# Optimization experiments

Hardware: AMD Instinct MI355X
Metric: run time of the kernel (lower is better)

The kernel has to match this reference:

```python
import jax, jax.numpy as jnp
import numpy as np

N = 50000
E = 800000
H = 128

def _mlp_init(key, sizes, bias_flags):
    ws = []
    for i, (din, dout) in enumerate(zip(sizes[:-1], sizes[1:])):
        key, k1, k2 = jax.random.split(key, 3)
        lim = 1.0 / np.sqrt(din)
        W = jax.random.uniform(k1, (din, dout), jnp.float32, -lim, lim)
        ws.append(W)
        if bias_flags[i]:
            ws.append(jax.random.uniform(k2, (dout,), jnp.float32, -lim, lim))
    return key, ws

def setup_inputs() -> dict:
    key = jax.random.key(0)
    key, kh, kx, ke = jax.random.split(key, 4)
    h = jax.random.normal(kh, (N, H), jnp.float32)
    x = jax.random.normal(kx, (N, 3), jnp.float32)
    edge_index = jax.random.randint(ke, (2, E), 0, N, jnp.int64)
    # edge_mlp: Linear(2H+1, H), Linear(H, H), both with bias
    key, (W_e1, b_e1, W_e2, b_e2) = _mlp_init(key, [2 * H + 1, H, H], [True, True])
    # coord_mlp: Linear(H, H) with bias, Linear(H, 1) no bias
    key, (W_c1, b_c1, W_c2) = _mlp_init(key, [H, H, 1], [True, False])
    # node_mlp: Linear(2H, H), Linear(H, H), both with bias
    key, (W_n1, b_n1, W_n2, b_n2) = _mlp_init(key, [2 * H, H, H], [True, True])
    ln_g = jnp.ones((H,), jnp.float32)
    ln_b = jnp.zeros((H,), jnp.float32)
    return {"h": h, "x": x, "edge_index": edge_index,
            "W_e1": W_e1, "b_e1": b_e1, "W_e2": W_e2, "b_e2": b_e2,
            "W_c1": W_c1, "b_c1": b_c1, "W_c2": W_c2,
            "W_n1": W_n1, "b_n1": b_n1, "W_n2": W_n2, "b_n2": b_n2,
            "ln_g": ln_g, "ln_b": ln_b}

def reference(h, x, edge_index, W_e1, b_e1, W_e2, b_e2, W_c1, b_c1, W_c2,
              W_n1, b_n1, W_n2, b_n2, ln_g, ln_b):
    row, col = edge_index[0], edge_index[1]
    coord_diff = x[row] - x[col]                       # [E, 3]
    dist = jnp.linalg.norm(coord_diff, axis=1, keepdims=True)  # [E, 1]
    radial = dist ** 2
    edge_input = jnp.concatenate([h[row], h[col], radial], axis=1)  # [E, 2H+1]
    m_ij = jax.nn.silu(jax.nn.silu(edge_input @ W_e1 + b_e1) @ W_e2 + b_e2)  # [E, H]
    force_scalar = jnp.tanh(jax.nn.silu(m_ij @ W_c1 + b_c1) @ W_c2) * 0.1    # [E, 1]
    norm_diff = coord_diff / (dist + 1e-8)
    force_vector = norm_diff * force_scalar            # [E, 3]
    x_new = x + jax.ops.segment_sum(force_vector, row, num_segments=N)
    m_i = jax.ops.segment_sum(m_ij, row, num_segments=N)  # [N, H]
    node_input = jnp.concatenate([h, m_i], axis=1)     # [N, 2H]
    h_res = h + jax.nn.silu(node_input @ W_n1 + b_n1) @ W_n2 + b_n2
    mu = jnp.mean(h_res, axis=-1, keepdims=True)
    var = jnp.var(h_res, axis=-1, keepdims=True)
    h_new = (h_res - mu) / jnp.sqrt(var + 1e-5) * ln_g + ln_b
    return (h_new, x_new)
```

## Files before the change

kernel.cpp:

```cpp
#include <hip/hip_runtime.h>
#include <hip/hip_bf16.h>

#define NN 50000
#define NE 800000
#define HH 128
#define SCAN_NB 196

typedef short s16x8 __attribute__((ext_vector_type(8)));
typedef float f32x4 __attribute__((ext_vector_type(4)));
typedef unsigned int u32x4 __attribute__((ext_vector_type(4)));
typedef __bf16 bf16x2 __attribute__((ext_vector_type(2)));

__device__ __forceinline__ float u2f(unsigned int v) {
    float f;
    __builtin_memcpy(&f, &v, 4);
    return f;
}
__device__ __forceinline__ float bf2f(unsigned short u) {
    return u2f(((unsigned int)u) << 16);
}
__device__ __forceinline__ unsigned short f2bf_sw(float f) {
    unsigned int x;
    __builtin_memcpy(&x, &f, 4);
    unsigned int r = (x + 0x7fffu + ((x >> 16) & 1u)) >> 16;
    return (unsigned short)r;
}
__device__ __forceinline__ unsigned int f2bf_pk(float a, float b) {
#if __has_builtin(__builtin_amdgcn_cvt_pk_bf16_f32)
    bf16x2 p = __builtin_amdgcn_cvt_pk_bf16_f32(a, b);
    unsigned int u;
    __builtin_memcpy(&u, &p, 4);
    return u;
#else
    return (unsigned int)f2bf_sw(a) | ((unsigned int)f2bf_sw(b) << 16);
#endif
}
__device__ __forceinline__ unsigned short f2bf(float a) {
#if __has_builtin(__builtin_amdgcn_cvt_pk_bf16_f32)
    return (unsigned short)(f2bf_pk(a, a) & 0xffffu);
#else
    return f2bf_sw(a);
#endif
}
__device__ __forceinline__ float silu(float v) {
    return v * __builtin_amdgcn_rcpf(1.f + __expf(-v));
}

__global__ void prep_kernel(
    const float* __restrict__ W_e1, const float* __restrict__ W_e2,
    const float* __restrict__ W_c1, const float* __restrict__ W_n1,
    const float* __restrict__ W_n2, const int* __restrict__ eidx,
    unsigned short* __restrict__ PWT, unsigned short* __restrict__ W2T,
    unsigned short* __restrict__ Wc1T, unsigned short* __restrict__ Wn1T,
    unsigned short* __restrict__ Wn2T, int* __restrict__ counts) {
    int idx = blockIdx.x * 256 + threadIdx.x;
    if (idx < 32768) {
        int cp = idx >> 7, k = idx & 127;
        int srow = (cp < 128) ? k : (128 + k);
        PWT[idx] = f2bf(W_e1[srow * 128 + (cp & 127)]);
    } else if (idx < 49152) {
        int i = idx - 32768, n = i >> 7, k = i & 127;
        W2T[i] = f2bf(W_e2[k * 128 + n]);
    } else if (idx < 65536) {
        int i = idx - 49152, n = i >> 7, k = i & 127;
        Wc1T[i] = f2bf(W_c1[k * 128 + n]);
    } else if (idx < 98304) {
        int i = idx - 65536, n = i >> 8, k = i & 255;
        Wn1T[i] = f2bf(W_n1[k * 128 + n]);
    } else if (idx < 114688) {
        int i = idx - 98304, n = i >> 7, k = i & 127;
        Wn2T[i] = f2bf(W_n2[k * 128 + n]);
    } else if (idx < 114688 + NE) {
        int e = idx - 114688;
        int r = eidx[e];
        r = r < 0 ? 0 : (r >= NN ? NN - 1 : r);
        atomicAdd(&counts[r], 1);
    }
}

__global__ void k_partial(const int* __restrict__ counts, int* __restrict__ partials) {
    __shared__ int sm[256];
    int idx = blockIdx.x * 256 + threadIdx.x;
    sm[threadIdx.x] = idx < NN ? counts[idx] : 0;
    __syncthreads();
    for (int s = 128; s > 0; s >>= 1) {
        if (threadIdx.x < s) sm[threadIdx.x] += sm[threadIdx.x + s];
        __syncthreads();
    }
    if (threadIdx.x == 0) partials[blockIdx.x] = sm[0];
}
__global__ void k_scanp(const int* __restrict__ partials, int* __restrict__ scanp) {
    __shared__ int sm[256];
    int t = threadIdx.x;
    int v = t < SCAN_NB ? partials[t] : 0;
    sm[t] = v;
    __syncthreads();
    for (int d = 1; d < 256; d <<= 1) {
        int add = t >= d ? sm[t - d] : 0;
        __syncthreads();
        sm[t] += add;
        __syncthreads();
    }
    scanp[t] = sm[t] - v;
}
__global__ void k_offsets(const int* __restrict__ counts, const int* __restrict__ scanp,
                          int* __restrict__ offsets) {
    __shared__ int sm[256];
    int t = threadIdx.x, idx = blockIdx.x * 256 + t;
    int v = idx < NN ? counts[idx] : 0;
    sm[t] = v;
    __syncthreads();
    for (int d = 1; d < 256; d <<= 1) {
        int add = t >= d ? sm[t - d] : 0;
        __syncthreads();
        sm[t] += add;
        __syncthreads();
    }
    if (idx < NN) offsets[idx] = sm[t] - v + scanp[blockIdx.x];
}

__global__ void k_fill(const int* __restrict__ eidx, const int* __restrict__ offsets,
                       int* __restrict__ cursor, unsigned int* __restrict__ rc) {
    int e = blockIdx.x * 256 + threadIdx.x;
    if (e >= NE) return;
    int r = eidx[e];
    int c = eidx[NE + e];
    r = r < 0 ? 0 : (r >= NN ? NN - 1 : r);
    c = c < 0 ? 0 : (c >= NN ? NN - 1 : c);
    int slot = offsets[r] + atomicAdd(&cursor[r], 1);
    rc[slot] = (unsigned int)r | ((unsigned int)c << 16);
}

__global__ __launch_bounds__(256, 4) void pgemm(
    const float* __restrict__ h, const unsigned short* __restrict__ PWT,
    const float* __restrict__ b1,
    float* __restrict__ P1, float* __restrict__ P2) {
    __shared__ unsigned short Alds[64 * 136];
    const int tid = threadIdx.x;
    const int n0 = blockIdx.x * 64;

#pragma unroll
    for (int j = 0; j < 4; j++) {
        int idx = tid + j * 256;
        int e = idx >> 4, ch = idx & 15;
        int node = n0 + e;
        if (node >= NN) node = NN - 1;
        const f32x4* p = (const f32x4*)&h[node * 128 + ch * 8];
        f32x4 a = p[0], b = p[1];
        u32x4 s;
        s[0] = f2bf_pk(a[0], a[1]);
        s[1] = f2bf_pk(a[2], a[3]);
        s[2] = f2bf_pk(b[0], b[1]);
        s[3] = f2bf_pk(b[2], b[3]);
        *(u32x4*)&Alds[e * 136 + ch * 8] = s;
    }
    __syncthreads();

    const int lane = tid & 63;
    const int w = tid >> 6;
    const int ln15 = lane & 15;
    const int q8 = (lane >> 4) * 8, q4 = (lane >> 4) * 4;
    const int cbase = w * 64;

    f32x4 acc[4][4];
#pragma unroll
    for (int et = 0; et < 4; et++)
#pragma unroll
        for (int nt = 0; nt < 4; nt++) acc[et][nt] = (f32x4){0.f, 0.f, 0.f, 0.f};
#pragma unroll
    for (int kk = 0; kk < 4; kk++) {
        int k0 = kk * 32 + q8;
        s16x8 a[4], b[4];
#pragma unroll
        for (int et = 0; et < 4; et++)
            a[et] = *(const s16x8*)&Alds[(et * 16 + ln15) * 136 + k0];
#pragma unroll
        for (int nt = 0; nt < 4; nt++)
            b[nt] = *(const s16x8*)&PWT[(cbase + nt * 16 + ln15) * 128 + k0];
#pragma unroll
        for (int et = 0; et < 4; et++)
#pragma unroll
            for (int nt = 0; nt < 4; nt++)
                acc[et][nt] = __builtin_amdgcn_mfma_f32_16x16x32_bf16(
                    a[et], b[nt], acc[et][nt], 0, 0, 0);
    }
#pragma unroll
    for (int nt = 0; nt < 4; nt++) {
        int cp = cbase + nt * 16 + ln15;
        bool top = cp < 128;
        float* dst = top ? P1 : P2;
        int col = cp & 127;
        float badd = top ? b1[col] : 0.f;
#pragma unroll
        for (int et = 0; et < 4; et++)
#pragma unroll
            for (int r = 0; r < 4; r++) {
                int row = et * 16 + q4 + r;
                int node = n0 + row;
                if (node >= NN) node = NN - 1;
                dst[(size_t)node * 128 + col] = acc[et][nt][r] + badd;
            }
    }
}

__global__ __launch_bounds__(256, 8) void edge_kernel(
    const float* __restrict__ P1, const float* __restrict__ P2,
    const float* __restrict__ x, const unsigned int* __restrict__ rc,
    const float* __restrict__ W1full,
    const unsigned short* __restrict__ W2T, const float* __restrict__ b2,
    const unsigned short* __restrict__ Wc1T, const float* __restrict__ bc1,
    const float* __restrict__ wc2,
    float* __restrict__ m_i, float* __restrict__ x_acc) {
    __shared__ unsigned short mid1[64 * 132];
    __shared__ float wls[128];
    __shared__ float rad[64], ndx[64], ndy[64], ndz[64], fsum[64];
    __shared__ int rowA[64], colA[64];

    const int tid = threadIdx.x;
    const int e0 = blockIdx.x * 64;

    if (tid < 64) {
        unsigned int pk = rc[e0 + tid];
        int r = pk & 0xffff, c = pk >> 16;
        rowA[tid] = r; colA[tid] = c;
        float dx = x[r * 3 + 0] - x[c * 3 + 0];
        float dy = x[r * 3 + 1] - x[c * 3 + 1];
        float dz = x[r * 3 + 2] - x[c * 3 + 2];
        float d2 = dx * dx + dy * dy + dz * dz;
        float dist = sqrtf(d2);
        float inv = __builtin_amdgcn_rcpf(dist + 1e-8f);
        rad[tid] = d2;
        ndx[tid] = dx * inv; ndy[tid] = dy * inv; ndz[tid] = dz * inv;
        fsum[tid] = 0.f;
    } else if (tid >= 128 && tid < 256) {
        int c = tid - 128;
        wls[c] = W1full[256 * 128 + c];
    }
    __syncthreads();

#pragma unroll
    for (int j = 0; j < 4; j++) {
        int idx = tid + j * 256;
        int e = idx >> 4, ch = idx & 15;
        int r = rowA[e], c = colA[e];
        const f32x4* q1 = (const f32x4*)&P1[(size_t)r * 128 + ch * 8];
        const f32x4* q2 = (const f32x4*)&P2[(size_t)c * 128 + ch * 8];
        f32x4 a0 = q1[0], a1 = q1[1];
        f32x4 c0 = q2[0], c1 = q2[1];
        float rd = rad[e];
        int colb = ch * 8;
        u32x4 s;
#pragma unroll
        for (int t = 0; t < 2; t++) {
            float v0 = a0[t * 2] + c0[t * 2] + rd * wls[colb + t * 2];
            float v1 = a0[t * 2 + 1] + c0[t * 2 + 1] + rd * wls[colb + t * 2 + 1];
            s[t] = f2bf_pk(silu(v0), silu(v1));
        }
#pragma unroll
        for (int t = 0; t < 2; t++) {
            int cc = colb + 4 + t * 2;
            float v0 = a1[t * 2] + c1[t * 2] + rd * wls[cc];
            float v1 = a1[t * 2 + 1] + c1[t * 2 + 1] + rd * wls[cc + 1];
            s[t + 2] = f2bf_pk(silu(v0), silu(v1));
        }
        *(u32x4*)&mid1[e * 132 + ch * 8] = s;
    }
    __syncthreads();

    const int lane = tid & 63;
    const int w = tid >> 6;
    const int ln15 = lane & 15;
    const int q8 = (lane >> 4) * 8, q4 = (lane >> 4) * 4;
    const int nbase = w * 32;

    f32x4 acc[4][2];

#pragma unroll
    for (int et = 0; et < 4; et++)
#pragma unroll
        for (int nt = 0; nt < 2; nt++) acc[et][nt] = (f32x4){0.f, 0.f, 0.f, 0.f};
#pragma unroll
    for (int kk = 0; kk < 4; kk++) {
        int k0 = kk * 32 + q8;
        s16x8 a[4], b[2];
#pragma unroll
        for (int et = 0; et < 4; et++)
            a[et] = *(const s16x8*)&mid1[(et * 16 + ln15) * 132 + k0];
#pragma unroll
        for (int nt = 0; nt < 2; nt++)
            b[nt] = *(const s16x8*)&W2T[(nbase + nt * 16 + ln15) * 128 + k0];
#pragma unroll
        for (int et = 0; et < 4; et++)
#pragma unroll
            for (int nt = 0; nt < 2; nt++)
                acc[et][nt] = __builtin_amdgcn_mfma_f32_16x16x32_bf16(
                    a[et], b[nt], acc[et][nt], 0, 0, 0);
    }
    __syncthreads();
    unsigned short* mid2 = mid1;
#pragma unroll
    for (int nt = 0; nt < 2; nt++) {
        int col = nbase + nt * 16 + ln15;
        float bias = b2[col];
#pragma unroll
        for (int et = 0; et < 4; et++)
#pragma unroll
            for (int r = 0; r < 4; r++) {
                int row = et * 16 + q4 + r;
                mid2[row * 132 + col] = f2bf(silu(acc[et][nt][r] + bias));
            }
    }
    __syncthreads();

#pragma unroll
    for (int et = 0; et < 4; et++)
#pragma unroll
        for (int nt = 0; nt < 2; nt++) acc[et][nt] = (f32x4){0.f, 0.f, 0.f, 0.f};
#pragma unroll
    for (int kk = 0; kk < 4; kk++) {
        int k0 = kk * 32 + q8;
        s16x8 a[4], b[2];
#pragma unroll
        for (int et = 0; et < 4; et++)
            a[et] = *(const s16x8*)&mid2[(et * 16 + ln15) * 132 + k0];
#pragma unroll
        for (int nt = 0; nt < 2; nt++)
            b[nt] = *(const s16x8*)&Wc1T[(nbase + nt * 16 + ln15) * 128 + k0];
#pragma unroll
        for (int et = 0; et < 4; et++)
#pragma unroll
            for (int nt = 0; nt < 2; nt++)
                acc[et][nt] = __builtin_amdgcn_mfma_f32_16x16x32_bf16(
                    a[et], b[nt], acc[et][nt], 0, 0, 0);
    }

    {
        int cp2 = (tid & 63) * 2;
        int g = tid >> 6;
        int r0 = g * 16;
        float a0 = 0.f, a1 = 0.f;
        int cur = rowA[r0];
        for (int row = r0; row < r0 + 16; row++) {
            int rn = rowA[row];
            if (rn != cur) {
                atomicAdd(&m_i[(size_t)cur * 128 + cp2], a0);
                atomicAdd(&m_i[(size_t)cur * 128 + cp2 + 1], a1);
                a0 = 0.f; a1 = 0.f;
                cur = rn;
            }
            unsigned int v = *(const unsigned int*)&mid2[row * 132 + cp2];
            a0 += u2f(v << 16);
            a1 += u2f(v & 0xffff0000u);
        }
        atomicAdd(&m_i[(size_t)cur * 128 + cp2], a0);
        atomicAdd(&m_i[(size_t)cur * 128 + cp2 + 1], a1);
    }

    {
        float part[4][4];
#pragma unroll
        for (int et = 0; et < 4; et++)
#pragma unroll
            for (int r = 0; r < 4; r++) part[et][r] = 0.f;
#pragma unroll
        for (int nt = 0; nt < 2; nt++) {
            int col = nbase + nt * 16 + ln15;
            float bias = bc1[col];
            float w2 = wc2[col];
#pragma unroll
            for (int et = 0; et < 4; et++)
#pragma unroll
                for (int r = 0; r < 4; r++)
                    part[et][r] += silu(acc[et][nt][r] + bias) * w2;
        }
#pragma unroll
        for (int et = 0; et < 4; et++)
#pragma unroll
            for (int r = 0; r < 4; r++) {
                float p = part[et][r];
                p += __shfl_xor(p, 8, 16);
                p += __shfl_xor(p, 4, 16);
                p += __shfl_xor(p, 2, 16);
                p += __shfl_xor(p, 1, 16);
                if (ln15 == 0) atomicAdd(&fsum[et * 16 + q4 + r], p);
            }
    }
    __syncthreads();
    if (tid < 64) {
        float fs = tanhf(fsum[tid]) * 0.1f;
        ndx[tid] *= fs; ndy[tid] *= fs; ndz[tid] *= fs;
    }
    __syncthreads();
    if (tid < 64) {
        bool head = (tid == 0) || (rowA[tid] != rowA[tid - 1]);
        if (head) {
            int rn = rowA[tid];
            float ax = 0.f, ay = 0.f, az = 0.f;
            for (int j = tid; j < 64 && rowA[j] == rn; j++) {
                ax += ndx[j]; ay += ndy[j]; az += ndz[j];
            }
            atomicAdd(&x_acc[rn * 3 + 0], ax);
            atomicAdd(&x_acc[rn * 3 + 1], ay);
            atomicAdd(&x_acc[rn * 3 + 2], az);
        }
    }
}

__global__ __launch_bounds__(256, 4) void node_kernel(
    const float* __restrict__ h, const float* __restrict__ m_i,
    const float* __restrict__ x, const float* __restrict__ x_acc,
    const unsigned short* __restrict__ Wn1T, const float* __restrict__ bn1,
    const unsigned short* __restrict__ Wn2T, const float* __restrict__ bn2,
    const float* __restrict__ ln_g, const float* __restrict__ ln_b,
    float* __restrict__ out_h, float* __restrict__ out_x) {
    __shared__ unsigned short Alds[64 * 264];
    unsigned short* mid1 = Alds;
    float* tile = (float*)Alds;

    const int tid = threadIdx.x;
    const int n0 = blockIdx.x * 64;

    if (tid < 192) {
        int i = n0 * 3 + tid;
        if (i < NN * 3) out_x[i] = x[i] + x_acc[i];
    }

#pragma unroll
    for (int i = 0; i < 8; i++) {
        int idx = tid + i * 256;
        int hr = idx >> 4, ch = idx & 15;
        int e = hr >> 1, half = hr & 1;
        int node = n0 + e;
        if (node >= NN) node = NN - 1;
        const float* src = half ? &m_i[(size_t)node * 128 + ch * 8]
                                : &h[(size_t)node * 128 + ch * 8];
        const f32x4* sp = (const f32x4*)src;
        f32x4 f0 = sp[0], f1 = sp[1];
        u32x4 s;
        s[0] = f2bf_pk(f0[0], f0[1]);
        s[1] = f2bf_pk(f0[2], f0[3]);
        s[2] = f2bf_pk(f1[0], f1[1]);
        s[3] = f2bf_pk(f1[2], f1[3]);
        *(u32x4*)&Alds[e * 264 + half * 128 + ch * 8] = s;
    }
    __syncthreads();

    const int lane = tid & 63;
    const int w = tid >> 6;
    const int ln15 = lane & 15;
    const int q8 = (lane >> 4) * 8, q4 = (lane >> 4) * 4;
    const int nbase = w * 32;

    f32x4 acc[4][2];

#pragma unroll
    for (int et = 0; et < 4; et++)
#pragma unroll
        for (int nt = 0; nt < 2; nt++) acc[et][nt] = (f32x4){0.f, 0.f, 0.f, 0.f};
#pragma unroll
    for (int kk = 0; kk < 8; kk++) {
        int k0 = kk * 32 + q8;
        s16x8 a[4], b[2];
#pragma unroll
        for (int et = 0; et < 4; et++)
            a[et] = *(const s16x8*)&Alds[(et * 16 + ln15) * 264 + k0];
#pragma unroll
        for (int nt = 0; nt < 2; nt++)
            b[nt] = *(const s16x8*)&Wn1T[(nbase + nt * 16 + ln15) * 256 + k0];
#pragma unroll
        for (int et = 0; et < 4; et++)
#pragma unroll
            for (int nt = 0; nt < 2; nt++)
                acc[et][nt] = __builtin_amdgcn_mfma_f32_16x16x32_bf16(
                    a[et], b[nt], acc[et][nt], 0, 0, 0);
    }
    __syncthreads();
#pragma unroll
    for (int nt = 0; nt < 2; nt++) {
        int col = nbase + nt * 16 + ln15;
        float bias = bn1[col];
#pragma unroll
        for (int et = 0; et < 4; et++)
#pragma unroll
            for (int r = 0; r < 4; r++) {
                int row = et * 16 + q4 + r;
                mid1[row * 132 + col] = f2bf(silu(acc[et][nt][r] + bias));
            }
    }
    __syncthreads();

#pragma unroll
    for (int et = 0; et < 4; et++)
#pragma unroll
        for (int nt = 0; nt < 2; nt++) acc[et][nt] = (f32x4){0.f, 0.f, 0.f, 0.f};
#pragma unroll
    for (int kk = 0; kk < 4; kk++) {
        int k0 = kk * 32 + q8;
        s16x8 a[4], b[2];
#pragma unroll
        for (int et = 0; et < 4; et++)
            a[et] = *(const s16x8*)&mid1[(et * 16 + ln15) * 132 + k0];
#pragma unroll
        for (int nt = 0; nt < 2; nt++)
            b[nt] = *(const s16x8*)&Wn2T[(nbase + nt * 16 + ln15) * 128 + k0];
#pragma unroll
        for (int et = 0; et < 4; et++)
#pragma unroll
            for (int nt = 0; nt < 2; nt++)
                acc[et][nt] = __builtin_amdgcn_mfma_f32_16x16x32_bf16(
                    a[et], b[nt], acc[et][nt], 0, 0, 0);
    }
    __syncthreads();
#pragma unroll
    for (int nt = 0; nt < 2; nt++) {
        int col = nbase + nt * 16 + ln15;
        float bias = bn2[col];
#pragma unroll
        for (int et = 0; et < 4; et++)
#pragma unroll
            for (int r = 0; r < 4; r++) {
                int row = et * 16 + q4 + r;
                int node = n0 + row;
                int nclamp = node >= NN ? NN - 1 : node;
                float v = acc[et][nt][r] + bias + h[(size_t)nclamp * 128 + col];
                tile[row * 132 + col] = v;
            }
    }
    __syncthreads();

    {
        int row = tid >> 2;
        int q = tid & 3;
        float s = 0.f, s2 = 0.f;
#pragma unroll
        for (int c = 0; c < 32; c++) {
            float v = tile[row * 132 + q + c * 4];
            s += v; s2 += v * v;
        }
        s += __shfl_xor(s, 1, 4);  s2 += __shfl_xor(s2, 1, 4);
        s += __shfl_xor(s, 2, 4);  s2 += __shfl_xor(s2, 2, 4);
        float mean = s * (1.f / 128.f);
        float var = s2 * (1.f / 128.f) - mean * mean;
        float rs = rsqrtf(var + 1e-5f);
        int node = n0 + row;
        if (node < NN) {
#pragma unroll
            for (int c = 0; c < 32; c++) {
                int col = q + c * 4;
                float v = (tile[row * 132 + col] - mean) * rs * ln_g[col] + ln_b[col];
                out_h[(size_t)node * 128 + col] = v;
            }
        }
    }
}

extern "C" void kernel_launch(void* const* d_in, const int* in_sizes, int n_in,
                              void* d_out, int out_size, void* d_ws, size_t ws_size,
                              hipStream_t stream) {
    const float* h    = (const float*)d_in[0];
    const float* x    = (const float*)d_in[1];
    const int* eidx   = (const int*)d_in[2];
    const float* W_e1 = (const float*)d_in[3];
    const float* b_e1 = (const float*)d_in[4];
    const float* W_e2 = (const float*)d_in[5];
    const float* b_e2 = (const float*)d_in[6];
    const float* W_c1 = (const float*)d_in[7];
    const float* b_c1 = (const float*)d_in[8];
    const float* W_c2 = (const float*)d_in[9];
    const float* W_n1 = (const float*)d_in[10];
    const float* b_n1 = (const float*)d_in[11];
    const float* W_n2 = (const float*)d_in[12];
    const float* b_n2 = (const float*)d_in[13];
    const float* ln_g = (const float*)d_in[14];
    const float* ln_b = (const float*)d_in[15];

    float* out_h = (float*)d_out;
    float* out_x = out_h + NN * HH;

    char* ws = (char*)d_ws;
    float* m_i    = (float*)ws;
    float* x_acc  = (float*)(ws + 25600000);
    int* counts   = (int*)(ws + 26200000);
    int* cursor   = (int*)(ws + 26400000);
    int* offsets  = (int*)(ws + 26600000);
    int* partials = (int*)(ws + 26800000);
    int* scanp    = (int*)(ws + 26801024);
    unsigned int* rc = (unsigned int*)(ws + 26802048);
    float* P1 = (float*)(ws + 30002048);
    float* P2 = (float*)(ws + 55602048);
    unsigned short* PWT  = (unsigned short*)(ws + 81202048);
    unsigned short* W2T  = (unsigned short*)(ws + 81267584);
    unsigned short* Wc1T = (unsigned short*)(ws + 81300352);
    unsigned short* Wn1T = (unsigned short*)(ws + 81333120);
    unsigned short* Wn2T = (unsigned short*)(ws + 81398656);

    hipMemsetAsync(ws, 0, 26800000, stream);

    prep_kernel<<<(114688 + NE + 255) / 256, 256, 0, stream>>>(
        W_e1, W_e2, W_c1, W_n1, W_n2, eidx, PWT, W2T, Wc1T, Wn1T, Wn2T, counts);
    k_partial<<<SCAN_NB, 256, 0, stream>>>(counts, partials);
    k_scanp<<<1, 256, 0, stream>>>(partials, scanp);
    k_offsets<<<SCAN_NB, 256, 0, stream>>>(counts, scanp, offsets);
    k_fill<<<(NE + 255) / 256, 256, 0, stream>>>(eidx, offsets, cursor, rc);
    pgemm<<<(NN + 63) / 64, 256, 0, stream>>>(h, PWT, b_e1, P1, P2);

    edge_kernel<<<NE / 64, 256, 0, stream>>>(P1, P2, x, rc, W_e1, W2T, b_e2,
                                             Wc1T, b_c1, W_c2, m_i, x_acc);
    node_kernel<<<(NN + 63) / 64, 256, 0, stream>>>(
        h, m_i, x, x_acc, Wn1T, b_n1, Wn2T, b_n2, ln_g, ln_b, out_h, out_x);
}
```

Before: 433.9 us.

## Store P2 in bf16, fuse scan kernels, shrink node tiles, rework edge reductions

Stores the col-side projection P2 as bf16 instead of fp32, halving the bytes gathered per edge in the edge kernel. It also merges the partial-scan kernel into the offsets kernel, so each block reduces the preceding partials itself and one launch is dropped. The segmented m_i reduction now uses one column per thread over 32 rows, and the force accumulation uses a wavefront shuffle segmented scan instead of a serial head loop. The node kernel uses 32-node tiles with higher occupancy bounds. Rounding P2 to bf16 adds precision loss to the first edge-layer preactivation.

```diff
diff --git a/kernel.cpp b/kernel.cpp
--- a/kernel.cpp
+++ b/kernel.cpp
@@ -89,10 +89,22 @@
     }
     if (threadIdx.x == 0) partials[blockIdx.x] = sm[0];
 }
-__global__ void k_scanp(const int* __restrict__ partials, int* __restrict__ scanp) {
+__global__ void k_offsets(const int* __restrict__ counts,
+                          const int* __restrict__ partials,
+                          int* __restrict__ offsets) {
     __shared__ int sm[256];
-    int t = threadIdx.x;
-    int v = t < SCAN_NB ? partials[t] : 0;
+    int t = threadIdx.x, bid = blockIdx.x;
+    int pv = (t < bid) ? partials[t] : 0;
+    sm[t] = pv;
+    __syncthreads();
+    for (int s = 128; s > 0; s >>= 1) {
+        if (t < s) sm[t] += sm[t + s];
+        __syncthreads();
+    }
+    int base = sm[0];
+    __syncthreads();
+    int idx = bid * 256 + t;
+    int v = idx < NN ? counts[idx] : 0;
     sm[t] = v;
     __syncthreads();
     for (int d = 1; d < 256; d <<= 1) {
@@ -101,22 +113,7 @@
         sm[t] += add;
         __syncthreads();
     }
-    scanp[t] = sm[t] - v;
-}
-__global__ void k_offsets(const int* __restrict__ counts, const int* __restrict__ scanp,
-                          int* __restrict__ offsets) {
-    __shared__ int sm[256];
-    int t = threadIdx.x, idx = blockIdx.x * 256 + t;
-    int v = idx < NN ? counts[idx] : 0;
-    sm[t] = v;
-    __syncthreads();
-    for (int d = 1; d < 256; d <<= 1) {
-        int add = t >= d ? sm[t - d] : 0;
-        __syncthreads();
-        sm[t] += add;
-        __syncthreads();
-    }
-    if (idx < NN) offsets[idx] = sm[t] - v + scanp[blockIdx.x];
+    if (idx < NN) offsets[idx] = sm[t] - v + base;
 }
 
 __global__ void k_fill(const int* __restrict__ eidx, const int* __restrict__ offsets,
@@ -134,7 +131,7 @@
 __global__ __launch_bounds__(256, 4) void pgemm(
     const float* __restrict__ h, const unsigned short* __restrict__ PWT,
     const float* __restrict__ b1,
-    float* __restrict__ P1, float* __restrict__ P2) {
+    float* __restrict__ P1, unsigned short* __restrict__ P2) {
     __shared__ unsigned short Alds[64 * 136];
     const int tid = threadIdx.x;
     const int n0 = blockIdx.x * 64;
@@ -187,24 +184,32 @@
 #pragma unroll
     for (int nt = 0; nt < 4; nt++) {
         int cp = cbase + nt * 16 + ln15;
-        bool top = cp < 128;
-        float* dst = top ? P1 : P2;
         int col = cp & 127;
-        float badd = top ? b1[col] : 0.f;
-#pragma unroll
-        for (int et = 0; et < 4; et++)
-#pragma unroll
-            for (int r = 0; r < 4; r++) {
-                int row = et * 16 + q4 + r;
-                int node = n0 + row;
-                if (node >= NN) node = NN - 1;
-                dst[(size_t)node * 128 + col] = acc[et][nt][r] + badd;
-            }
+        if (cp < 128) {
+            float badd = b1[col];
+#pragma unroll
+            for (int et = 0; et < 4; et++)
+#pragma unroll
+                for (int r = 0; r < 4; r++) {
+                    int node = n0 + et * 16 + q4 + r;
+                    if (node >= NN) node = NN - 1;
+                    P1[(size_t)node * 128 + col] = acc[et][nt][r] + badd;
+                }
+        } else {
+#pragma unroll
+            for (int et = 0; et < 4; et++)
+#pragma unroll
+                for (int r = 0; r < 4; r++) {
+                    int node = n0 + et * 16 + q4 + r;
+                    if (node >= NN) node = NN - 1;
+                    P2[(size_t)node * 128 + col] = f2bf(acc[et][nt][r]);
+                }
+        }
     }
 }
 
 __global__ __launch_bounds__(256, 8) void edge_kernel(
-    const float* __restrict__ P1, const float* __restrict__ P2,
+    const float* __restrict__ P1, const unsigned short* __restrict__ P2,
     const float* __restrict__ x, const unsigned int* __restrict__ rc,
     const float* __restrict__ W1full,
     const unsigned short* __restrict__ W2T, const float* __restrict__ b2,
@@ -244,23 +249,24 @@
         int e = idx >> 4, ch = idx & 15;
         int r = rowA[e], c = colA[e];
         const f32x4* q1 = (const f32x4*)&P1[(size_t)r * 128 + ch * 8];
-        const f32x4* q2 = (const f32x4*)&P2[(size_t)c * 128 + ch * 8];
         f32x4 a0 = q1[0], a1 = q1[1];
-        f32x4 c0 = q2[0], c1 = q2[1];
+        u32x4 p2 = *(const u32x4*)&P2[(size_t)c * 128 + ch * 8];
         float rd = rad[e];
         int colb = ch * 8;
         u32x4 s;
 #pragma unroll
         for (int t = 0; t < 2; t++) {
-            float v0 = a0[t * 2] + c0[t * 2] + rd * wls[colb + t * 2];
-            float v1 = a0[t * 2 + 1] + c0[t * 2 + 1] + rd * wls[colb + t * 2 + 1];
+            float c0 = u2f(p2[t] << 16), c1 = u2f(p2[t] & 0xffff0000u);
+            float v0 = a0[t * 2] + c0 + rd * wls[colb + t * 2];
+            float v1 = a0[t * 2 + 1] + c1 + rd * wls[colb + t * 2 + 1];
             s[t] = f2bf_pk(silu(v0), silu(v1));
         }
 #pragma unroll
         for (int t = 0; t < 2; t++) {
             int cc = colb + 4 + t * 2;
-            float v0 = a1[t * 2] + c1[t * 2] + rd * wls[cc];
-            float v1 = a1[t * 2 + 1] + c1[t * 2 + 1] + rd * wls[cc + 1];
+            float c0 = u2f(p2[t + 2] << 16), c1 = u2f(p2[t + 2] & 0xffff0000u);
+            float v0 = a1[t * 2] + c0 + rd * wls[cc];
+            float v1 = a1[t * 2 + 1] + c1 + rd * wls[cc + 1];
             s[t + 2] = f2bf_pk(silu(v0), silu(v1));
         }
         *(u32x4*)&mid1[e * 132 + ch * 8] = s;
@@ -335,25 +341,20 @@
     }
 
     {
-        int cp2 = (tid & 63) * 2;
-        int g = tid >> 6;
-        int r0 = g * 16;
-        float a0 = 0.f, a1 = 0.f;
+        int col = tid & 127;
+        int r0 = (tid >> 7) * 32;
+        float accv = 0.f;
         int cur = rowA[r0];
-        for (int row = r0; row < r0 + 16; row++) {
+        for (int row = r0; row < r0 + 32; row++) {
             int rn = rowA[row];
             if (rn != cur) {
-                atomicAdd(&m_i[(size_t)cur * 128 + cp2], a0);
-                atomicAdd(&m_i[(size_t)cur * 128 + cp2 + 1], a1);
-                a0 = 0.f; a1 = 0.f;
+                atomicAdd(&m_i[(size_t)cur * 128 + col], accv);
+                accv = 0.f;
                 cur = rn;
             }
-            unsigned int v = *(const unsigned int*)&mid2[row * 132 + cp2];
-            a0 += u2f(v << 16);
-            a1 += u2f(v & 0xffff0000u);
-        }
-        atomicAdd(&m_i[(size_t)cur * 128 + cp2], a0);
-        atomicAdd(&m_i[(size_t)cur * 128 + cp2 + 1], a1);
+            accv += bf2f(mid2[row * 132 + col]);
+        }
+        atomicAdd(&m_i[(size_t)cur * 128 + col], accv);
     }
 
     {
@@ -388,45 +389,46 @@
     __syncthreads();
     if (tid < 64) {
         float fs = tanhf(fsum[tid]) * 0.1f;
-        ndx[tid] *= fs; ndy[tid] *= fs; ndz[tid] *= fs;
-    }
-    __syncthreads();
-    if (tid < 64) {
-        bool head = (tid == 0) || (rowA[tid] != rowA[tid - 1]);
-        if (head) {
-            int rn = rowA[tid];
-            float ax = 0.f, ay = 0.f, az = 0.f;
-            for (int j = tid; j < 64 && rowA[j] == rn; j++) {
-                ax += ndx[j]; ay += ndy[j]; az += ndz[j];
-            }
-            atomicAdd(&x_acc[rn * 3 + 0], ax);
-            atomicAdd(&x_acc[rn * 3 + 1], ay);
-            atomicAdd(&x_acc[rn * 3 + 2], az);
-        }
-    }
-}
-
-__global__ __launch_bounds__(256, 4) void node_kernel(
+        float ax = ndx[tid] * fs, ay = ndy[tid] * fs, az = ndz[tid] * fs;
+        int myrow = rowA[tid];
+#pragma unroll
+        for (int d = 1; d < 64; d <<= 1) {
+            float px = __shfl_up(ax, d, 64);
+            float py = __shfl_up(ay, d, 64);
+            float pz = __shfl_up(az, d, 64);
+            int pr = __shfl_up(myrow, d, 64);
+            if (tid >= d && pr == myrow) { ax += px; ay += py; az += pz; }
+        }
+        int nrow = __shfl_down(myrow, 1, 64);
+        if (tid == 63 || nrow != myrow) {
+            atomicAdd(&x_acc[myrow * 3 + 0], ax);
+            atomicAdd(&x_acc[myrow * 3 + 1], ay);
+            atomicAdd(&x_acc[myrow * 3 + 2], az);
+        }
+    }
+}
+
+__global__ __launch_bounds__(256, 8) void node_kernel(
     const float* __restrict__ h, const float* __restrict__ m_i,
     const float* __restrict__ x, const float* __restrict__ x_acc,
     const unsigned short* __restrict__ Wn1T, const float* __restrict__ bn1,
     const unsigned short* __restrict__ Wn2T, const float* __restrict__ bn2,
     const float* __restrict__ ln_g, const float* __restrict__ ln_b,
     float* __restrict__ out_h, float* __restrict__ out_x) {
-    __shared__ unsigned short Alds[64 * 264];
+    __shared__ unsigned short Alds[32 * 264];
     unsigned short* mid1 = Alds;
     float* tile = (float*)Alds;
 
     const int tid = threadIdx.x;
-    const int n0 = blockIdx.x * 64;
-
-    if (tid < 192) {
+    const int n0 = blockIdx.x * 32;
+
+    if (tid < 96) {
         int i = n0 * 3 + tid;
         if (i < NN * 3) out_x[i] = x[i] + x_acc[i];
     }
 
 #pragma unroll
-    for (int i = 0; i < 8; i++) {
+    for (int i = 0; i < 4; i++) {
         int idx = tid + i * 256;
         int hr = idx >> 4, ch = idx & 15;
         int e = hr >> 1, half = hr & 1;
@@ -451,24 +453,24 @@
     const int q8 = (lane >> 4) * 8, q4 = (lane >> 4) * 4;
     const int nbase = w * 32;
 
-    f32x4 acc[4][2];
-
-#pragma unroll
-    for (int et = 0; et < 4; et++)
+    f32x4 acc[2][2];
+
+#pragma unroll
+    for (int et = 0; et < 2; et++)
 #pragma unroll
         for (int nt = 0; nt < 2; nt++) acc[et][nt] = (f32x4){0.f, 0.f, 0.f, 0.f};
 #pragma unroll
     for (int kk = 0; kk < 8; kk++) {
         int k0 = kk * 32 + q8;
-        s16x8 a[4], b[2];
-#pragma unroll
-        for (int et = 0; et < 4; et++)
+        s16x8 a[2], b[2];
+#pragma unroll
+        for (int et = 0; et < 2; et++)
             a[et] = *(const s16x8*)&Alds[(et * 16 + ln15) * 264 + k0];
 #pragma unroll
         for (int nt = 0; nt < 2; nt++)
             b[nt] = *(const s16x8*)&Wn1T[(nbase + nt * 16 + ln15) * 256 + k0];
 #pragma unroll
-        for (int et = 0; et < 4; et++)
+        for (int et = 0; et < 2; et++)
 #pragma unroll
             for (int nt = 0; nt < 2; nt++)
                 acc[et][nt] = __builtin_amdgcn_mfma_f32_16x16x32_bf16(
@@ -480,7 +482,7 @@
         int col = nbase + nt * 16 + ln15;
         float bias = bn1[col];
 #pragma unroll
-        for (int et = 0; et < 4; et++)
+        for (int et = 0; et < 2; et++)
 #pragma unroll
             for (int r = 0; r < 4; r++) {
                 int row = et * 16 + q4 + r;
@@ -490,21 +492,21 @@
     __syncthreads();
 
 #pragma unroll
-    for (int et = 0; et < 4; et++)
+    for (int et = 0; et < 2; et++)
 #pragma unroll
         for (int nt = 0; nt < 2; nt++) acc[et][nt] = (f32x4){0.f, 0.f, 0.f, 0.f};
 #pragma unroll
     for (int kk = 0; kk < 4; kk++) {
         int k0 = kk * 32 + q8;
-        s16x8 a[4], b[2];
-#pragma unroll
-        for (int et = 0; et < 4; et++)
+        s16x8 a[2], b[2];
+#pragma unroll
+        for (int et = 0; et < 2; et++)
             a[et] = *(const s16x8*)&mid1[(et * 16 + ln15) * 132 + k0];
 #pragma unroll
         for (int nt = 0; nt < 2; nt++)
             b[nt] = *(const s16x8*)&Wn2T[(nbase + nt * 16 + ln15) * 128 + k0];
 #pragma unroll
-        for (int et = 0; et < 4; et++)
+        for (int et = 0; et < 2; et++)
 #pragma unroll
             for (int nt = 0; nt < 2; nt++)
                 acc[et][nt] = __builtin_amdgcn_mfma_f32_16x16x32_bf16(
@@ -516,7 +518,7 @@
         int col = nbase + nt * 16 + ln15;
         float bias = bn2[col];
 #pragma unroll
-        for (int et = 0; et < 4; et++)
+        for (int et = 0; et < 2; et++)
 #pragma unroll
             for (int r = 0; r < 4; r++) {
                 int row = et * 16 + q4 + r;
@@ -529,24 +531,25 @@
     __syncthreads();
 
     {
-        int row = tid >> 2;
-        int q = tid & 3;
+        int row = tid >> 3;
+        int q = tid & 7;
         float s = 0.f, s2 = 0.f;
 #pragma unroll
-        for (int c = 0; c < 32; c++) {
-            float v = tile[row * 132 + q + c * 4];
+        for (int c = 0; c < 16; c++) {
+            float v = tile[row * 132 + q + c * 8];
             s += v; s2 += v * v;
         }
-        s += __shfl_xor(s, 1, 4);  s2 += __shfl_xor(s2, 1, 4);
-        s += __shfl_xor(s, 2, 4);  s2 += __shfl_xor(s2, 2, 4);
+        s += __shfl_xor(s, 1, 8);  s2 += __shfl_xor(s2, 1, 8);
+        s += __shfl_xor(s, 2, 8);  s2 += __shfl_xor(s2, 2, 8);
+        s += __shfl_xor(s, 4, 8);  s2 += __shfl_xor(s2, 4, 8);
         float mean = s * (1.f / 128.f);
         float var = s2 * (1.f / 128.f) - mean * mean;
         float rs = rsqrtf(var + 1e-5f);
         int node = n0 + row;
         if (node < NN) {
 #pragma unroll
-            for (int c = 0; c < 32; c++) {
-                int col = q + c * 4;
+            for (int c = 0; c < 16; c++) {
+                int col = q + c * 8;
                 float v = (tile[row * 132 + col] - mean) * rs * ln_g[col] + ln_b[col];
                 out_h[(size_t)node * 128 + col] = v;
             }
@@ -584,28 +587,26 @@
     int* cursor   = (int*)(ws + 26400000);
     int* offsets  = (int*)(ws + 26600000);
     int* partials = (int*)(ws + 26800000);
-    int* scanp    = (int*)(ws + 26801024);
     unsigned int* rc = (unsigned int*)(ws + 26802048);
     float* P1 = (float*)(ws + 30002048);
-    float* P2 = (float*)(ws + 55602048);
-    unsigned short* PWT  = (unsigned short*)(ws + 81202048);
-    unsigned short* W2T  = (unsigned short*)(ws + 81267584);
-    unsigned short* Wc1T = (unsigned short*)(ws + 81300352);
-    unsigned short* Wn1T = (unsigned short*)(ws + 81333120);
-    unsigned short* Wn2T = (unsigned short*)(ws + 81398656);
+    unsigned short* P2 = (unsigned short*)(ws + 55602048);
+    unsigned short* PWT  = (unsigned short*)(ws + 68402048);
+    unsigned short* W2T  = (unsigned short*)(ws + 68467584);
+    unsigned short* Wc1T = (unsigned short*)(ws + 68500352);
+    unsigned short* Wn1T = (unsigned short*)(ws + 68533120);
+    unsigned short* Wn2T = (unsigned short*)(ws + 68598656);
 
     hipMemsetAsync(ws, 0, 26800000, stream);
 
     prep_kernel<<<(114688 + NE + 255) / 256, 256, 0, stream>>>(
         W_e1, W_e2, W_c1, W_n1, W_n2, eidx, PWT, W2T, Wc1T, Wn1T, Wn2T, counts);
     k_partial<<<SCAN_NB, 256, 0, stream>>>(counts, partials);
-    k_scanp<<<1, 256, 0, stream>>>(partials, scanp);
-    k_offsets<<<SCAN_NB, 256, 0, stream>>>(counts, scanp, offsets);
+    k_offsets<<<SCAN_NB, 256, 0, stream>>>(counts, partials, offsets);
     k_fill<<<(NE + 255) / 256, 256, 0, stream>>>(eidx, offsets, cursor, rc);
     pgemm<<<(NN + 63) / 64, 256, 0, stream>>>(h, PWT, b_e1, P1, P2);
 
     edge_kernel<<<NE / 64, 256, 0, stream>>>(P1, P2, x, rc, W_e1, W2T, b_e2,
                                              Wc1T, b_c1, W_c2, m_i, x_acc);
-    node_kernel<<<(NN + 63) / 64, 256, 0, stream>>>(
+    node_kernel<<<(NN + 31) / 32, 256, 0, stream>>>(
         h, m_i, x, x_acc, Wn1T, b_n1, Wn2T, b_n2, ln_g, ln_b, out_h, out_x);
 }
```

After: 436.2 us. Within noise of the previous version (+0.5%).
